# Optimization experiments

Measured on AMD Instinct MI355X. Metric: run time of the kernel, lower is better.

## Reference

```python
import jax, jax.numpy as jnp
import numpy as np

C = 64          # channels
HEADS = 4       # num_heads -> head_dim = 16
HID = int(C * 2.66)  # 170, GDFN hidden channels
B, H, W = 2, 256, 256


def conv1x1(x, w):
    # x: (b,c,h,w), w: (o,c) -> pointwise conv, no bias
    return jnp.einsum('bchw,oc->bohw', x, w)


def dwconv3x3(x, w):
    # depthwise 3x3, SAME padding; w: (C,1,3,3)
    return jax.lax.conv_general_dilated(
        x, w, window_strides=(1, 1), padding='SAME',
        feature_group_count=x.shape[1],
        dimension_numbers=('NCHW', 'OIHW', 'NCHW'))


def layer_norm_c(x, w, b):
    # torch: LayerNorm over channel dim of (b, hw, c), eps=1e-5
    mu = x.mean(axis=1, keepdims=True)
    var = ((x - mu) ** 2).mean(axis=1, keepdims=True)
    xn = (x - mu) / jnp.sqrt(var + 1e-5)
    return xn * w[None, :, None, None] + b[None, :, None, None]


def l2norm(x):
    # F.normalize(dim=-1), eps=1e-12
    n = jnp.sqrt(jnp.sum(x * x, axis=-1, keepdims=True))
    return x / jnp.maximum(n, 1e-12)


def mdta(x, temp, w_qkv, w_qkv_dw, w_po, w_kv, w_kv_dw, w_pof):
    b, c, h, w_ = x.shape
    d = c // HEADS
    qkv = dwconv3x3(conv1x1(x, w_qkv), w_qkv_dw)
    q, k, v = jnp.split(qkv, 3, axis=1)
    rs = lambda t: t.reshape(b, HEADS, d, h * w_)
    q, k, v = l2norm(rs(q)), l2norm(rs(k)), rs(v)
    # channel attention: (b,heads,d,d), softmax over last dim
    attn = jax.nn.softmax(jnp.einsum('bhdn,bhen->bhde', q, k) * temp, axis=-1)
    out = conv1x1(jnp.einsum('bhde,bhen->bhdn', attn, v).reshape(b, c, h, w_), w_po)
    # second gated branch: kv from `out`, reuse attn (qf/kf/attnf are dead code in source)
    kvf = dwconv3x3(conv1x1(out, w_kv), w_kv_dw)
    _kf, vf = jnp.split(kvf, 2, axis=1)
    vf = rs(vf)
    outf = conv1x1(jnp.einsum('bhde,bhen->bhdn', attn, vf).reshape(b, c, h, w_), w_pof)
    return outf


def gdfn(x, w_in, w_dw, w_out):
    x12 = dwconv3x3(conv1x1(x, w_in), w_dw)
    x1, x2 = jnp.split(x12, 2, axis=1)
    return conv1x1(jax.nn.gelu(x1, approximate=False) * x2, w_out)


def setup_inputs() -> dict:
    key = jax.random.key(0)
    ks = jax.random.split(key, 10)
    s = 0.05
    return {
        'x': jax.random.normal(ks[0], (B, C, H, W), jnp.float32),
        'n1_w': jnp.ones((C,), jnp.float32),
        'n1_b': jnp.zeros((C,), jnp.float32),
        'temp': jnp.ones((1, HEADS, 1, 1), jnp.float32),
        'w_qkv': jax.random.normal(ks[1], (3 * C, C), jnp.float32) * s,
        'w_qkv_dw': jax.random.normal(ks[2], (3 * C, 1, 3, 3), jnp.float32) * s,
        'w_po': jax.random.normal(ks[3], (C, C), jnp.float32) * s,
        'w_kv': jax.random.normal(ks[4], (2 * C, C), jnp.float32) * s,
        'w_kv_dw': jax.random.normal(ks[5], (2 * C, 1, 3, 3), jnp.float32) * s,
        'w_pof': jax.random.normal(ks[6], (C, C), jnp.float32) * s,
        'n2_w': jnp.ones((C,), jnp.float32),
        'n2_b': jnp.zeros((C,), jnp.float32),
        'w_in': jax.random.normal(ks[7], (2 * HID, C), jnp.float32) * s,
        'w_dw': jax.random.normal(ks[8], (2 * HID, 1, 3, 3), jnp.float32) * s,
        'w_out': jax.random.normal(ks[9], (C, HID), jnp.float32) * s,
    }


def reference(x, n1_w, n1_b, temp, w_qkv, w_qkv_dw, w_po, w_kv, w_kv_dw, w_pof,
              n2_w, n2_b, w_in, w_dw, w_out):
    x = x + mdta(layer_norm_c(x, n1_w, n1_b), temp,
                 w_qkv, w_qkv_dw, w_po, w_kv, w_kv_dw, w_pof)
    x = x + gdfn(layer_norm_c(x, n2_w, n2_b), w_in, w_dw, w_out)
    return x
```

## Files before the change

### kernel.cpp

```cpp
#include <hip/hip_runtime.h>
#include <hip/hip_bf16.h>
#include <math.h>

#define NPB 65536
#define BATCH 2
#define NTOT (BATCH * NPB)

typedef unsigned short u16;
typedef __attribute__((ext_vector_type(8))) short short8;
typedef __attribute__((ext_vector_type(4))) float f32x4;


__device__ __forceinline__ float bf2f(u16 u) {
  union { unsigned u; float f; } v; v.u = ((unsigned)u) << 16; return v.f;
}
__device__ __forceinline__ u16 f2bf(float f) {
  union { float f; unsigned u; } v; v.f = f;
  unsigned r = v.u + 0x7FFFu + ((v.u >> 16) & 1u);
  return (u16)(r >> 16);
}
__device__ __forceinline__ unsigned pk2(float a, float b) {
  return (unsigned)f2bf(a) | ((unsigned)f2bf(b) << 16);
}
__device__ __forceinline__ f32x4 mm(short8 a, short8 b, f32x4 c) {
  return __builtin_amdgcn_mfma_f32_16x16x32_bf16(a, b, c, 0, 0, 0);
}
__device__ __forceinline__ short8 ldfrag(const u16* F, int frag, int l) {
  return *reinterpret_cast<const short8*>(F + ((size_t)frag * 64 + l) * 8);
}
__device__ __forceinline__ void st4(u16* p, f32x4 c) {
  uint2 v; v.x = pk2(c[0], c[1]); v.y = pk2(c[2], c[3]);
  *reinterpret_cast<uint2*>(p) = v;
}
__device__ __forceinline__ float gelu_t(float a) {
  const float z = 0.7978845608f * fmaf(0.044715f * a, a * a, a);
  const float e = __expf(2.f * z);
  const float th = 1.f - 2.f / (e + 1.f);
  return 0.5f * a * (1.f + th);
}

__global__ __launch_bounds__(64) void k_wprep(
    const float* __restrict__ wqkv, const float* __restrict__ win,
    const float* __restrict__ wout, u16* __restrict__ WQf,
    u16* __restrict__ WIf, u16* __restrict__ WOf)
{
  const int f = blockIdx.x;
  const int l = threadIdx.x;
  const int fr = l & 15, fq = l >> 4;
  short8 v;
  u16* dst;
  if (f < 24) {
    const int t = f >> 1, kh = f & 1;
    const int row = t * 16 + fr;
#pragma unroll
    for (int j = 0; j < 8; ++j)
      v[j] = (short)f2bf(wqkv[(size_t)row * 64 + kh * 32 + fq * 8 + j]);
    dst = WQf + ((size_t)f * 64 + l) * 8;
  } else if (f < 68) {
    const int fi = f - 24;
    const int g = fi >> 1, kh = fi & 1;
    const int half = g / 11, t = g % 11;
    const int col = half * 176 + t * 16 + fr;
    const int row = col < 170 ? col : (col < 176 ? -1 : (col < 346 ? col - 6 : -1));
#pragma unroll
    for (int j = 0; j < 8; ++j)
      v[j] = (row < 0) ? (short)0
             : (short)f2bf(win[(size_t)row * 64 + kh * 32 + fq * 8 + j]);
    dst = WIf + ((size_t)fi * 64 + l) * 8;
  } else {
    const int fi = f - 68;
    const int t = fi / 6, kh = fi % 6;
    const int row = t * 16 + fr;
#pragma unroll
    for (int j = 0; j < 8; ++j) {
      const int k = kh * 32 + fq * 8 + j;
      v[j] = (k < 170) ? (short)f2bf(wout[(size_t)row * 170 + k]) : (short)0;
    }
    dst = WOf + ((size_t)fi * 64 + l) * 8;
  }
  *reinterpret_cast<short8*>(dst) = v;
}

__global__ __launch_bounds__(256, 4) void k_ln1(
    const float* __restrict__ x, const float* __restrict__ n1w,
    const float* __restrict__ n1b, u16* __restrict__ Y1)
{
  const int n = blockIdx.x * 256 + threadIdx.x;
  const int b = blockIdx.y;
  const size_t pix = (size_t)b * NPB + n;
  const float* xb = x + ((size_t)b * 64) * NPB + n;
  float y[64];
  float mu = 0.f;
#pragma unroll
  for (int c = 0; c < 64; ++c) { y[c] = xb[(size_t)c * NPB]; mu += y[c]; }
  mu *= (1.f / 64.f);
  float var = 0.f;
#pragma unroll
  for (int c = 0; c < 64; ++c) { float d = y[c] - mu; var = fmaf(d, d, var); }
  const float rstd = rsqrtf(var * (1.f / 64.f) + 1e-5f);
#pragma unroll
  for (int c = 0; c < 64; ++c) y[c] = (y[c] - mu) * rstd * n1w[c] + n1b[c];
#pragma unroll
  for (int cb = 0; cb < 4; ++cb) {
    u16* dst = Y1 + ((size_t)cb * NTOT + pix) * 16;
    uint4 v0, v1;
    v0.x = pk2(y[cb*16+0],  y[cb*16+1]);  v0.y = pk2(y[cb*16+2],  y[cb*16+3]);
    v0.z = pk2(y[cb*16+4],  y[cb*16+5]);  v0.w = pk2(y[cb*16+6],  y[cb*16+7]);
    v1.x = pk2(y[cb*16+8],  y[cb*16+9]);  v1.y = pk2(y[cb*16+10], y[cb*16+11]);
    v1.z = pk2(y[cb*16+12], y[cb*16+13]); v1.w = pk2(y[cb*16+14], y[cb*16+15]);
    *reinterpret_cast<uint4*>(dst) = v0;
    *reinterpret_cast<uint4*>(dst + 8) = v1;
  }
}

__global__ __launch_bounds__(256, 2) void g_qkvp(
    const u16* __restrict__ Y1, const u16* __restrict__ WQf,
    u16* __restrict__ qkvp)
{
  const int l = threadIdx.x & 63, fr = l & 15, fq = l >> 4;
  const int wv = blockIdx.x * 4 + (threadIdx.x >> 6);
  const int nw = gridDim.x * 4;
  short8 A[12][2];
#pragma unroll
  for (int t = 0; t < 12; ++t)
#pragma unroll
    for (int kh = 0; kh < 2; ++kh) A[t][kh] = ldfrag(WQf, t * 2 + kh, l);
  const size_t hof = (size_t)(fq & 1) * 8;
  for (int tile = wv; tile < 8192; tile += nw) {
    const size_t n = (size_t)tile * 16 + fr;
    const short8 b0 = *reinterpret_cast<const short8*>(
        Y1 + (((size_t)(fq >> 1)) * NTOT + n) * 16 + hof);
    const short8 b1 = *reinterpret_cast<const short8*>(
        Y1 + (((size_t)(2 + (fq >> 1))) * NTOT + n) * 16 + hof);
    f32x4 c[12];
#pragma unroll
    for (int t = 0; t < 12; ++t) c[t] = f32x4{0.f, 0.f, 0.f, 0.f};
#pragma unroll
    for (int t = 0; t < 12; ++t) c[t] = mm(A[t][0], b0, c[t]);
#pragma unroll
    for (int t = 0; t < 12; ++t) c[t] = mm(A[t][1], b1, c[t]);
#pragma unroll
    for (int t = 0; t < 12; ++t)
      st4(qkvp + ((size_t)t * NTOT + n) * 16 + fq * 4, c[t]);
  }
}

template<int CH, bool GATE, int STRIP>
__global__ __launch_bounds__(256, 2) void k_dwr(
    const u16* __restrict__ in, u16* __restrict__ out,
    const float* __restrict__ wdw, int wofs)
{
  typedef short __attribute__((ext_vector_type(CH))) shortC;
  constexpr int NPL = GATE ? 2 : 1;
  constexpr int LPP = 16 / CH;
  constexpr int NX  = 256 / LPP;
  constexpr int XC  = 256 / NX;
  const int t = threadIdx.x;
  const int sub = t % LPP, xi = t / LPP;
  const int q = blockIdx.x / XC, xc = blockIdx.x % XC;
  const int strip = blockIdx.y, b = blockIdx.z;
  const int x = xc * NX + xi;
  const int y0 = strip * STRIP;
  const int e0 = sub * CH;
  const int c0 = q * 16 + e0;

  const u16* pin[NPL];
  pin[0] = in + ((size_t)q * NTOT + (size_t)b * NPB) * 16 + e0;
  if (GATE)
    pin[NPL - 1] = in + ((size_t)(11 + q) * NTOT + (size_t)b * NPB) * 16 + e0;

  float w[NPL][9][CH];
#pragma unroll
  for (int pl = 0; pl < NPL; ++pl)
#pragma unroll
    for (int ch = 0; ch < CH; ++ch) {
      const int c = c0 + ch;
      int row; bool valid;
      if (GATE) { valid = c < 170; row = pl * 170 + c; }
      else { valid = true; row = wofs + c; }
#pragma unroll
      for (int tap = 0; tap < 9; ++tap)
        w[pl][tap][ch] = valid ? wdw[(size_t)row * 9 + tap] : 0.f;
    }

  auto LD = [&](const u16* p, int yy, int xx) -> shortC {
    shortC v;
#pragma unroll
    for (int j = 0; j < CH; ++j) v[j] = 0;
    if ((unsigned)yy < 256u && (unsigned)xx < 256u)
      v = *reinterpret_cast<const shortC*>(p + (size_t)(yy * 256 + xx) * 16);
    return v;
  };

  shortC r[NPL][3][3];
#pragma unroll
  for (int pl = 0; pl < NPL; ++pl) {
    r[pl][0][0] = LD(pin[pl], y0 - 1, x - 1);
    r[pl][0][1] = LD(pin[pl], y0 - 1, x);
    r[pl][0][2] = LD(pin[pl], y0 - 1, x + 1);
    r[pl][1][0] = LD(pin[pl], y0, x - 1);
    r[pl][1][1] = LD(pin[pl], y0, x);
    r[pl][1][2] = LD(pin[pl], y0, x + 1);
  }

#pragma unroll 2
  for (int yy = 0; yy < STRIP; ++yy) {
    const int y = y0 + yy;
#pragma unroll
    for (int pl = 0; pl < NPL; ++pl) {
      r[pl][2][0] = LD(pin[pl], y + 1, x - 1);
      r[pl][2][1] = LD(pin[pl], y + 1, x);
      r[pl][2][2] = LD(pin[pl], y + 1, x + 1);
    }
    float acc[NPL][CH];
#pragma unroll
    for (int pl = 0; pl < NPL; ++pl)
#pragma unroll
      for (int ch = 0; ch < CH; ++ch) acc[pl][ch] = 0.f;
#pragma unroll
    for (int pl = 0; pl < NPL; ++pl)
#pragma unroll
      for (int ky = 0; ky < 3; ++ky)
#pragma unroll
        for (int kx = 0; kx < 3; ++kx)
#pragma unroll
          for (int ch = 0; ch < CH; ++ch)
            acc[pl][ch] = fmaf(w[pl][ky * 3 + kx][ch],
                               bf2f((u16)r[pl][ky][kx][ch]), acc[pl][ch]);

    float v[CH];
#pragma unroll
    for (int ch = 0; ch < CH; ++ch) {
      if (GATE) {
        v[ch] = gelu_t(acc[0][ch]) * acc[NPL - 1][ch];
      } else {
        v[ch] = acc[0][ch];
      }
    }
    u16* po = out + ((size_t)q * NTOT + (size_t)b * NPB +
                     (size_t)(y * 256 + x)) * 16 + e0;
    if constexpr (CH == 4) {
      uint2 o; o.x = pk2(v[0], v[1]); o.y = pk2(v[2], v[3]);
      *reinterpret_cast<uint2*>(po) = o;
    } else {
      uint4 o;
      o.x = pk2(v[0], v[1]); o.y = pk2(v[2], v[3]);
      o.z = pk2(v[4], v[5]); o.w = pk2(v[6], v[7]);
      *reinterpret_cast<uint4*>(po) = o;
    }
#pragma unroll
    for (int pl = 0; pl < NPL; ++pl)
#pragma unroll
      for (int dx = 0; dx < 3; ++dx) {
        r[pl][0][dx] = r[pl][1][dx];
        r[pl][1][dx] = r[pl][2][dx];
      }
  }
}

__global__ __launch_bounds__(256, 2) void k_gram_p(
    const u16* __restrict__ qkv, float* __restrict__ part)
{
  __shared__ __align__(16) u16 lds[32][520];
  const int chunk = blockIdx.x, h = blockIdx.y, b = blockIdx.z;
  const int t = threadIdx.x;
#pragma unroll
  for (int i = 0; i < 2; ++i) {
    const int p = t + i * 256;
    const size_t pix = (size_t)b * NPB + chunk * 512 + p;
    const u16* srcq = qkv + ((size_t)h * NTOT + pix) * 16;
    const u16* srck = qkv + ((size_t)(4 + h) * NTOT + pix) * 16;
    const short8 q0 = *reinterpret_cast<const short8*>(srcq);
    const short8 q1 = *reinterpret_cast<const short8*>(srcq + 8);
    const short8 k0 = *reinterpret_cast<const short8*>(srck);
    const short8 k1 = *reinterpret_cast<const short8*>(srck + 8);
#pragma unroll
    for (int j = 0; j < 8; ++j) {
      lds[j][p] = (u16)q0[j];  lds[8 + j][p] = (u16)q1[j];
      lds[16 + j][p] = (u16)k0[j]; lds[24 + j][p] = (u16)k1[j];
    }
  }
  __syncthreads();
  const int w = t >> 6, l = t & 63, fr = l & 15, fq = l >> 4;
  if (w >= 3) return;
  float* pp = part + ((size_t)((b * 4 + h) * 128) + chunk) * 288;
  const int rowA = (w == 2) ? 16 + fr : fr;
  const int rowB = (w == 0) ? 16 + fr : rowA;
  f32x4 acc = {0.f, 0.f, 0.f, 0.f};
#pragma unroll
  for (int kt = 0; kt < 16; ++kt) {
    const short8 a  = *reinterpret_cast<const short8*>(&lds[rowA][kt * 32 + fq * 8]);
    const short8 bb = *reinterpret_cast<const short8*>(&lds[rowB][kt * 32 + fq * 8]);
    acc = mm(a, bb, acc);
  }
  if (w == 0) {
#pragma unroll
    for (int r = 0; r < 4; ++r) pp[(fq * 4 + r) * 16 + fr] = acc[r];
  } else if ((fr >> 2) == fq) {
    pp[(w == 1 ? 256 : 272) + fr] = acc[fr & 3];
  }
}

__global__ __launch_bounds__(320) void k_gram_red(
    const float* __restrict__ part, float* __restrict__ G,
    float* __restrict__ Sq, float* __restrict__ Sk)
{
  const int bh = blockIdx.x;
  const int t = threadIdx.x;
  if (t >= 288) return;
  const float* p = part + (size_t)bh * 128 * 288 + t;
  float s = 0.f;
  for (int ch = 0; ch < 128; ++ch) s += p[(size_t)ch * 288];
  const int b = bh >> 2, h = bh & 3;
  if (t < 256) G[bh * 256 + t] = s;
  else if (t < 272) Sq[b * 64 + h * 16 + (t - 256)] = s;
  else Sk[b * 64 + h * 16 + (t - 272)] = s;
}

__global__ __launch_bounds__(256) void k_attn(
    const float* __restrict__ G, const float* __restrict__ Sq,
    const float* __restrict__ Sk, const float* __restrict__ temp,
    const float* __restrict__ wpo, const float* __restrict__ wkv,
    const float* __restrict__ wpof, u16* __restrict__ Pf,
    u16* __restrict__ M2f)
{
  __shared__ float attn[BATCH][4][16][16];
  __shared__ float M1[BATCH][64][64];
  __shared__ float rq[128], rk[128];
  const int t = threadIdx.x;
  if (t < 128) {
    rq[t] = 1.f / fmaxf(sqrtf(Sq[t]), 1e-12f);
    rk[t] = 1.f / fmaxf(sqrtf(Sk[t]), 1e-12f);
  }
  __syncthreads();
  if (t < 128) {
    const int b = t >> 6, h = (t >> 4) & 3, d = t & 15;
    const float tm = temp[h];
    const float* g = G + ((b * 4 + h) * 16 + d) * 16;
    const float rqd = rq[b * 64 + h * 16 + d];
    float L[16], mx = -1e30f;
#pragma unroll
    for (int e = 0; e < 16; ++e) {
      L[e] = g[e] * rqd * rk[b * 64 + h * 16 + e] * tm;
      mx = fmaxf(mx, L[e]);
    }
    float s = 0.f;
#pragma unroll
    for (int e = 0; e < 16; ++e) { L[e] = expf(L[e] - mx); s += L[e]; }
    const float inv = 1.f / s;
#pragma unroll
    for (int e = 0; e < 16; ++e) attn[b][h][d][e] = L[e] * inv;
  }
  __syncthreads();
  for (int s0 = 0; s0 < 32; ++s0) {
    const int idx = t * 32 + s0;
    const int b = idx >> 12, o = (idx >> 6) & 63, c = idx & 63;
    const int h = c >> 4, e = c & 15;
    float a = 0.f;
#pragma unroll
    for (int d = 0; d < 16; ++d) a = fmaf(wpo[o * 64 + h * 16 + d], attn[b][h][d][e], a);
    M1[b][o][c] = a;
  }
  __syncthreads();
  for (int it = 0; it < 4; ++it) {
    const int idx = it * 256 + t;
    const int l = idx & 63;
    const int fi = idx >> 6;
    const int b = fi >> 3, tt = (fi >> 1) & 3, kh = fi & 1;
    const int fr = l & 15, fq = l >> 4;
    const int o = tt * 16 + fr;
    short8 pv, mv;
#pragma unroll
    for (int j = 0; j < 8; ++j) {
      const int c = kh * 32 + fq * 8 + j;
      const int h = c >> 4, e = c & 15;
      float a2 = 0.f;
#pragma unroll
      for (int d = 0; d < 16; ++d)
        a2 = fmaf(wpof[o * 64 + h * 16 + d], attn[b][h][d][e], a2);
      mv[j] = (short)f2bf(a2);
      float a = 0.f;
      for (int jj = 0; jj < 64; ++jj)
        a = fmaf(wkv[(64 + o) * 64 + jj], M1[b][jj][c], a);
      pv[j] = (short)f2bf(a);
    }
    *reinterpret_cast<short8*>(Pf + ((size_t)fi * 64 + l) * 8) = pv;
    *reinterpret_cast<short8*>(M2f + ((size_t)fi * 64 + l) * 8) = mv;
  }
}

__global__ __launch_bounds__(256, 2) void g_pv(
    const u16* __restrict__ qkv, const u16* __restrict__ Pf,
    u16* __restrict__ vfp)
{
  const int l = threadIdx.x & 63, fr = l & 15, fq = l >> 4;
  const int wv = blockIdx.x * 4 + (threadIdx.x >> 6);
  const int nw = gridDim.x * 4;
  const int b = blockIdx.z;
  short8 A[4][2];
#pragma unroll
  for (int t = 0; t < 4; ++t)
#pragma unroll
    for (int kh = 0; kh < 2; ++kh)
      A[t][kh] = ldfrag(Pf, (b * 4 + t) * 2 + kh, l);
  const size_t hof = (size_t)(fq & 1) * 8;
  for (int tile = wv; tile < 4096; tile += nw) {
    const size_t n = (size_t)b * NPB + (size_t)tile * 16 + fr;
    const short8 b0 = *reinterpret_cast<const short8*>(
        qkv + ((size_t)(8 + (fq >> 1)) * NTOT + n) * 16 + hof);
    const short8 b1 = *reinterpret_cast<const short8*>(
        qkv + ((size_t)(10 + (fq >> 1)) * NTOT + n) * 16 + hof);
    f32x4 c[4];
#pragma unroll
    for (int t = 0; t < 4; ++t) c[t] = f32x4{0.f, 0.f, 0.f, 0.f};
#pragma unroll
    for (int t = 0; t < 4; ++t) c[t] = mm(A[t][0], b0, c[t]);
#pragma unroll
    for (int t = 0; t < 4; ++t) c[t] = mm(A[t][1], b1, c[t]);
#pragma unroll
    for (int t = 0; t < 4; ++t)
      st4(vfp + ((size_t)t * NTOT + n) * 16 + fq * 4, c[t]);
  }
}

__global__ __launch_bounds__(256, 2) void g_x2ln(
    const u16* __restrict__ vf, const u16* __restrict__ M2f,
    const float* __restrict__ x, const float* __restrict__ n2w,
    const float* __restrict__ n2b, u16* __restrict__ X2,
    u16* __restrict__ Y2)
{
  const int l = threadIdx.x & 63, fr = l & 15, fq = l >> 4;
  const int wv = blockIdx.x * 4 + (threadIdx.x >> 6);
  const int nw = gridDim.x * 4;
  const int b = blockIdx.z;
  short8 A[4][2];
#pragma unroll
  for (int t = 0; t < 4; ++t)
#pragma unroll
    for (int kh = 0; kh < 2; ++kh)
      A[t][kh] = ldfrag(M2f, (b * 4 + t) * 2 + kh, l);
  const size_t hof = (size_t)(fq & 1) * 8;
  for (int tile = wv; tile < 4096; tile += nw) {
    const int pix0 = tile * 16;
    const size_t n = (size_t)b * NPB + pix0 + fr;
    const short8 b0 = *reinterpret_cast<const short8*>(
        vf + ((size_t)(fq >> 1) * NTOT + n) * 16 + hof);
    const short8 b1 = *reinterpret_cast<const short8*>(
        vf + ((size_t)(2 + (fq >> 1)) * NTOT + n) * 16 + hof);
    f32x4 c[4];
#pragma unroll
    for (int t = 0; t < 4; ++t) c[t] = f32x4{0.f, 0.f, 0.f, 0.f};
#pragma unroll
    for (int t = 0; t < 4; ++t) c[t] = mm(A[t][0], b0, c[t]);
#pragma unroll
    for (int t = 0; t < 4; ++t) c[t] = mm(A[t][1], b1, c[t]);
    const int pix = pix0 + fr;
#pragma unroll
    for (int t = 0; t < 4; ++t)
#pragma unroll
      for (int r = 0; r < 4; ++r)
        c[t][r] += x[((size_t)(b * 64 + t * 16 + fq * 4 + r)) * NPB + pix];
#pragma unroll
    for (int t = 0; t < 4; ++t)
      st4(X2 + ((size_t)t * NTOT + n) * 16 + fq * 4, c[t]);
    float s = 0.f;
#pragma unroll
    for (int t = 0; t < 4; ++t)
#pragma unroll
      for (int r = 0; r < 4; ++r) s += c[t][r];
    s += __shfl_xor(s, 16); s += __shfl_xor(s, 32);
    const float mu = s * (1.f / 64.f);
    float ss = 0.f;
#pragma unroll
    for (int t = 0; t < 4; ++t)
#pragma unroll
      for (int r = 0; r < 4; ++r) { float d = c[t][r] - mu; ss = fmaf(d, d, ss); }
    ss += __shfl_xor(ss, 16); ss += __shfl_xor(ss, 32);
    const float rstd = rsqrtf(ss * (1.f / 64.f) + 1e-5f);
#pragma unroll
    for (int t = 0; t < 4; ++t)
#pragma unroll
      for (int r = 0; r < 4; ++r) {
        const int oc = t * 16 + fq * 4 + r;
        c[t][r] = (c[t][r] - mu) * rstd * n2w[oc] + n2b[oc];
      }
#pragma unroll
    for (int t = 0; t < 4; ++t)
      st4(Y2 + ((size_t)t * NTOT + n) * 16 + fq * 4, c[t]);
  }
}

__global__ __launch_bounds__(256, 2) void g_win(
    const u16* __restrict__ Y2, const u16* __restrict__ WIf,
    u16* __restrict__ hpre)
{
  const int l = threadIdx.x & 63, fr = l & 15, fq = l >> 4;
  const int wv = blockIdx.x * 4 + (threadIdx.x >> 6);
  const int nw = gridDim.x * 4;
  const int half = wv & 1;
  short8 A[11][2];
#pragma unroll
  for (int t = 0; t < 11; ++t)
#pragma unroll
    for (int kh = 0; kh < 2; ++kh)
      A[t][kh] = ldfrag(WIf, (half * 11 + t) * 2 + kh, l);
  const size_t hof = (size_t)(fq & 1) * 8;
  for (int tile = wv >> 1; tile < 8192; tile += (nw >> 1)) {
    const size_t n = (size_t)tile * 16 + fr;
    const short8 b0 = *reinterpret_cast<const short8*>(
        Y2 + ((size_t)(fq >> 1) * NTOT + n) * 16 + hof);
    const short8 b1 = *reinterpret_cast<const short8*>(
        Y2 + ((size_t)(2 + (fq >> 1)) * NTOT + n) * 16 + hof);
    f32x4 c[11];
#pragma unroll
    for (int t = 0; t < 11; ++t) c[t] = f32x4{0.f, 0.f, 0.f, 0.f};
#pragma unroll
    for (int t = 0; t < 11; ++t) c[t] = mm(A[t][0], b0, c[t]);
#pragma unroll
    for (int t = 0; t < 11; ++t) c[t] = mm(A[t][1], b1, c[t]);
#pragma unroll
    for (int t = 0; t < 11; ++t)
      st4(hpre + ((size_t)(half * 11 + t) * NTOT + n) * 16 + fq * 4, c[t]);
  }
}

__global__ __launch_bounds__(256, 2) void g_out(
    const u16* __restrict__ hg, const u16* __restrict__ WOf,
    const u16* __restrict__ X2, float* __restrict__ out)
{
  const int l = threadIdx.x & 63, fr = l & 15, fq = l >> 4;
  const int wv = blockIdx.x * 4 + (threadIdx.x >> 6);
  const int nw = gridDim.x * 4;
  short8 A[4][6];
#pragma unroll
  for (int t = 0; t < 4; ++t)
#pragma unroll
    for (int kh = 0; kh < 6; ++kh)
      A[t][kh] = ldfrag(WOf, t * 6 + kh, l);
  const size_t hof = (size_t)(fq & 1) * 8;
  for (int tile = wv; tile < 8192; tile += nw) {
    const size_t n = (size_t)tile * 16 + fr;
    short8 bb[6];
#pragma unroll
    for (int kh = 0; kh < 6; ++kh) {
      int hb = kh * 2 + (fq >> 1);
      if (hb > 10) hb = 10;
      bb[kh] = *reinterpret_cast<const short8*>(
          hg + ((size_t)hb * NTOT + n) * 16 + hof);
    }
    f32x4 c[4];
#pragma unroll
    for (int t = 0; t < 4; ++t) c[t] = f32x4{0.f, 0.f, 0.f, 0.f};
#pragma unroll
    for (int kh = 0; kh < 6; ++kh)
#pragma unroll
      for (int t = 0; t < 4; ++t) c[t] = mm(A[t][kh], bb[kh], c[t]);
    const int b = (int)(n >> 16);
    const int pix = (int)(n & 65535);
#pragma unroll
    for (int t = 0; t < 4; ++t) {
      const uint2 xv = *reinterpret_cast<const uint2*>(
          X2 + ((size_t)t * NTOT + n) * 16 + fq * 4);
      const u16 h0 = (u16)(xv.x & 0xffff), h1 = (u16)(xv.x >> 16);
      const u16 h2 = (u16)(xv.y & 0xffff), h3 = (u16)(xv.y >> 16);
      const int ocb = b * 64 + t * 16 + fq * 4;
      out[((size_t)(ocb + 0)) * NPB + pix] = c[t][0] + bf2f(h0);
      out[((size_t)(ocb + 1)) * NPB + pix] = c[t][1] + bf2f(h1);
      out[((size_t)(ocb + 2)) * NPB + pix] = c[t][2] + bf2f(h2);
      out[((size_t)(ocb + 3)) * NPB + pix] = c[t][3] + bf2f(h3);
    }
  }
}

extern "C" void kernel_launch(void* const* d_in, const int* in_sizes, int n_in,
                              void* d_out, int out_size, void* d_ws, size_t ws_size,
                              hipStream_t stream)
{
  const float* x     = (const float*)d_in[0];
  const float* n1w   = (const float*)d_in[1];
  const float* n1b   = (const float*)d_in[2];
  const float* temp  = (const float*)d_in[3];
  const float* wqkv  = (const float*)d_in[4];
  const float* wqkvd = (const float*)d_in[5];
  const float* wpo   = (const float*)d_in[6];
  const float* wkv   = (const float*)d_in[7];
  const float* wkvd  = (const float*)d_in[8];
  const float* wpof  = (const float*)d_in[9];
  const float* n2w   = (const float*)d_in[10];
  const float* n2b   = (const float*)d_in[11];
  const float* win   = (const float*)d_in[12];
  const float* wdw   = (const float*)d_in[13];
  const float* wout  = (const float*)d_in[14];
  float* out = (float*)d_out;

  char* ws = (char*)d_ws;
  const size_t offA  = 0;
  const size_t offB  = 16777216;
  const size_t offC  = offB + 50331648;
  const size_t offHg = offC + 50331648;
  const size_t offX2 = offHg + 46137344 + 256;
  const size_t offSm = offX2 + 16777216;

  u16* Y1   = (u16*)(ws + offA);
  u16* VFP  = (u16*)(ws + offA);
  u16* Y2   = (u16*)(ws + offA);
  u16* QKVp = (u16*)(ws + offB);
  u16* VF   = (u16*)(ws + offB);
  u16* Hpre = (u16*)(ws + offB);
  u16* QKV  = (u16*)(ws + offC);
  u16* Hg   = (u16*)(ws + offHg);
  u16* X2   = (u16*)(ws + offX2);
  float* part = (float*)(ws + offSm);
  float* G    = (float*)(ws + offSm + 1179648);
  float* Sq   = (float*)(ws + offSm + 1179648 + 8192);
  float* Sk   = (float*)(ws + offSm + 1179648 + 8704);
  u16* Pf     = (u16*)(ws + offSm + 1179648 + 9216);
  u16* M2f    = (u16*)(ws + offSm + 1179648 + 25600);
  u16* WQf    = (u16*)(ws + offSm + 1179648 + 41984);
  u16* WIf    = (u16*)(ws + offSm + 1179648 + 66560);
  u16* WOf    = (u16*)(ws + offSm + 1179648 + 111616);

  k_wprep<<<dim3(92), 64, 0, stream>>>(wqkv, win, wout, WQf, WIf, WOf);
  k_ln1<<<dim3(NPB / 256, BATCH), 256, 0, stream>>>(x, n1w, n1b, Y1);
  g_qkvp<<<dim3(512), 256, 0, stream>>>(Y1, WQf, QKVp);
  k_dwr<8, false, 16><<<dim3(24, 16, BATCH), 256, 0, stream>>>(QKVp, QKV, wqkvd, 0);
  k_gram_p<<<dim3(128, 4, BATCH), 256, 0, stream>>>(QKV, part);
  k_gram_red<<<dim3(BATCH * 4), 320, 0, stream>>>(part, G, Sq, Sk);
  k_attn<<<dim3(1), 256, 0, stream>>>(G, Sq, Sk, temp, wpo, wkv, wpof, Pf, M2f);
  g_pv<<<dim3(256, 1, BATCH), 256, 0, stream>>>(QKV, Pf, VFP);
  k_dwr<8, false, 8><<<dim3(8, 32, BATCH), 256, 0, stream>>>(VFP, VF, wkvd, 64);
  g_x2ln<<<dim3(256, 1, BATCH), 256, 0, stream>>>(VF, M2f, x, n2w, n2b, X2, Y2);
  g_win<<<dim3(512), 256, 0, stream>>>(Y2, WIf, Hpre);
  k_dwr<4, true, 16><<<dim3(44, 16, BATCH), 256, 0, stream>>>(Hpre, Hg, wdw, 0);
  g_out<<<dim3(512), 256, 0, stream>>>(Hg, WOf, X2, out);
}
```

Before: 244.6 us.

## Fuse GDFN input 1x1 conv with depthwise 3x3 and GELU gate in LDS tiles

Replaces the separate g_win pointwise conv and gated depthwise conv kernels with one kernel. Each block loads a 16x16 spatial tile plus halo of Y2 into LDS, computes the hidden channels per 16-channel group with MFMA into LDS, then applies the 3x3 depthwise conv and GELU gate directly. This removes the large Hpre round trip through global memory (340 bf16 channels written then re-read with halo). In exchange it recomputes the halo pixels' pointwise conv, rounds depthwise weights to bf16, and uses a large LDS footprint, which may limit occupancy.

```diff
diff --git a/kernel.cpp b/kernel.cpp
--- a/kernel.cpp
+++ b/kernel.cpp
@@ -8,6 +8,7 @@
 
 typedef unsigned short u16;
 typedef __attribute__((ext_vector_type(8))) short short8;
+typedef __attribute__((ext_vector_type(4))) short short4v;
 typedef __attribute__((ext_vector_type(4))) float f32x4;
 
 
@@ -145,13 +146,12 @@
   }
 }
 
-template<int CH, bool GATE, int STRIP>
+template<int CH, int STRIP>
 __global__ __launch_bounds__(256, 2) void k_dwr(
     const u16* __restrict__ in, u16* __restrict__ out,
     const float* __restrict__ wdw, int wofs)
 {
   typedef short __attribute__((ext_vector_type(CH))) shortC;
-  constexpr int NPL = GATE ? 2 : 1;
   constexpr int LPP = 16 / CH;
   constexpr int NX  = 256 / LPP;
   constexpr int XC  = 256 / NX;
@@ -164,97 +164,161 @@
   const int e0 = sub * CH;
   const int c0 = q * 16 + e0;
 
-  const u16* pin[NPL];
-  pin[0] = in + ((size_t)q * NTOT + (size_t)b * NPB) * 16 + e0;
-  if (GATE)
-    pin[NPL - 1] = in + ((size_t)(11 + q) * NTOT + (size_t)b * NPB) * 16 + e0;
-
-  float w[NPL][9][CH];
-#pragma unroll
-  for (int pl = 0; pl < NPL; ++pl)
-#pragma unroll
-    for (int ch = 0; ch < CH; ++ch) {
-      const int c = c0 + ch;
-      int row; bool valid;
-      if (GATE) { valid = c < 170; row = pl * 170 + c; }
-      else { valid = true; row = wofs + c; }
-#pragma unroll
-      for (int tap = 0; tap < 9; ++tap)
-        w[pl][tap][ch] = valid ? wdw[(size_t)row * 9 + tap] : 0.f;
-    }
-
-  auto LD = [&](const u16* p, int yy, int xx) -> shortC {
+  const u16* pin = in + ((size_t)q * NTOT + (size_t)b * NPB) * 16 + e0;
+
+  float w[9][CH];
+#pragma unroll
+  for (int ch = 0; ch < CH; ++ch) {
+    const int row = wofs + c0 + ch;
+#pragma unroll
+    for (int tap = 0; tap < 9; ++tap)
+      w[tap][ch] = wdw[(size_t)row * 9 + tap];
+  }
+
+  auto LD = [&](int yy, int xx) -> shortC {
     shortC v;
 #pragma unroll
     for (int j = 0; j < CH; ++j) v[j] = 0;
     if ((unsigned)yy < 256u && (unsigned)xx < 256u)
-      v = *reinterpret_cast<const shortC*>(p + (size_t)(yy * 256 + xx) * 16);
+      v = *reinterpret_cast<const shortC*>(pin + (size_t)(yy * 256 + xx) * 16);
     return v;
   };
 
-  shortC r[NPL][3][3];
-#pragma unroll
-  for (int pl = 0; pl < NPL; ++pl) {
-    r[pl][0][0] = LD(pin[pl], y0 - 1, x - 1);
-    r[pl][0][1] = LD(pin[pl], y0 - 1, x);
-    r[pl][0][2] = LD(pin[pl], y0 - 1, x + 1);
-    r[pl][1][0] = LD(pin[pl], y0, x - 1);
-    r[pl][1][1] = LD(pin[pl], y0, x);
-    r[pl][1][2] = LD(pin[pl], y0, x + 1);
-  }
+  shortC r[3][3];
+  r[0][0] = LD(y0 - 1, x - 1); r[0][1] = LD(y0 - 1, x); r[0][2] = LD(y0 - 1, x + 1);
+  r[1][0] = LD(y0, x - 1);     r[1][1] = LD(y0, x);     r[1][2] = LD(y0, x + 1);
 
 #pragma unroll 2
   for (int yy = 0; yy < STRIP; ++yy) {
     const int y = y0 + yy;
-#pragma unroll
-    for (int pl = 0; pl < NPL; ++pl) {
-      r[pl][2][0] = LD(pin[pl], y + 1, x - 1);
-      r[pl][2][1] = LD(pin[pl], y + 1, x);
-      r[pl][2][2] = LD(pin[pl], y + 1, x + 1);
-    }
-    float acc[NPL][CH];
-#pragma unroll
-    for (int pl = 0; pl < NPL; ++pl)
-#pragma unroll
-      for (int ch = 0; ch < CH; ++ch) acc[pl][ch] = 0.f;
-#pragma unroll
-    for (int pl = 0; pl < NPL; ++pl)
-#pragma unroll
-      for (int ky = 0; ky < 3; ++ky)
-#pragma unroll
-        for (int kx = 0; kx < 3; ++kx)
-#pragma unroll
-          for (int ch = 0; ch < CH; ++ch)
-            acc[pl][ch] = fmaf(w[pl][ky * 3 + kx][ch],
-                               bf2f((u16)r[pl][ky][kx][ch]), acc[pl][ch]);
-
-    float v[CH];
-#pragma unroll
-    for (int ch = 0; ch < CH; ++ch) {
-      if (GATE) {
-        v[ch] = gelu_t(acc[0][ch]) * acc[NPL - 1][ch];
-      } else {
-        v[ch] = acc[0][ch];
-      }
-    }
+    r[2][0] = LD(y + 1, x - 1); r[2][1] = LD(y + 1, x); r[2][2] = LD(y + 1, x + 1);
+    float acc[CH];
+#pragma unroll
+    for (int ch = 0; ch < CH; ++ch) acc[ch] = 0.f;
+#pragma unroll
+    for (int ky = 0; ky < 3; ++ky)
+#pragma unroll
+      for (int kx = 0; kx < 3; ++kx)
+#pragma unroll
+        for (int ch = 0; ch < CH; ++ch)
+          acc[ch] = fmaf(w[ky * 3 + kx][ch], bf2f((u16)r[ky][kx][ch]), acc[ch]);
     u16* po = out + ((size_t)q * NTOT + (size_t)b * NPB +
                      (size_t)(y * 256 + x)) * 16 + e0;
-    if constexpr (CH == 4) {
+    uint4 o;
+    o.x = pk2(acc[0], acc[1]); o.y = pk2(acc[2], acc[3]);
+    o.z = pk2(acc[4], acc[5]); o.w = pk2(acc[6], acc[7]);
+    *reinterpret_cast<uint4*>(po) = o;
+#pragma unroll
+    for (int dx = 0; dx < 3; ++dx) { r[0][dx] = r[1][dx]; r[1][dx] = r[2][dx]; }
+  }
+}
+
+__global__ __launch_bounds__(256, 2) void g_windwg(
+    const u16* __restrict__ Y2, const u16* __restrict__ WIf,
+    const float* __restrict__ wdw, u16* __restrict__ Hg)
+{
+  __shared__ __align__(16) u16 sy[336 * 72];
+  __shared__ __align__(16) u16 sh[336 * 36];
+  __shared__ __align__(16) u16 swt[2 * 9 * 176];
+  const int t = threadIdx.x;
+  const int tx0 = blockIdx.x * 16, ty0 = blockIdx.y * 16;
+  const int b = blockIdx.z;
+  const size_t bofs = (size_t)b * NPB;
+
+  for (int i = t; i < 2 * 9 * 176; i += 256) {
+    const int pl = i / (9 * 176);
+    const int r = i % (9 * 176);
+    const int tap = r / 176, c = r % 176;
+    swt[i] = (c < 170) ? f2bf(wdw[((size_t)(pl * 170 + c)) * 9 + tap]) : (u16)0;
+  }
+  for (int idx = t; idx < 336; idx += 256) {
+    const int py = idx / 18, px = idx % 18;
+    const int gy = ty0 + py - 1, gx = tx0 + px - 1;
+    const bool ok = (idx < 324) && ((unsigned)gy < 256u) && ((unsigned)gx < 256u);
+#pragma unroll
+    for (int cb = 0; cb < 4; ++cb) {
+      short8 v0, v1;
+      if (ok) {
+        const u16* src = Y2 + ((size_t)cb * NTOT + bofs + (size_t)(gy * 256 + gx)) * 16;
+        v0 = *reinterpret_cast<const short8*>(src);
+        v1 = *reinterpret_cast<const short8*>(src + 8);
+      } else {
+#pragma unroll
+        for (int j = 0; j < 8; ++j) { v0[j] = 0; v1[j] = 0; }
+      }
+      *reinterpret_cast<short8*>(&sy[idx * 72 + cb * 16]) = v0;
+      *reinterpret_cast<short8*>(&sy[idx * 72 + cb * 16 + 8]) = v1;
+    }
+  }
+  __syncthreads();
+
+  const int w = t >> 6, l = t & 63, fr = l & 15, fq = l >> 4;
+  const int sub = t & 3, colx = (t >> 2) & 15, rg = t >> 6;
+  const int e0 = sub * 4;
+
+  for (int q = 0; q < 11; ++q) {
+    const short8 a10 = ldfrag(WIf, q * 2, l);
+    const short8 a11 = ldfrag(WIf, q * 2 + 1, l);
+    const short8 a20 = ldfrag(WIf, (11 + q) * 2, l);
+    const short8 a21 = ldfrag(WIf, (11 + q) * 2 + 1, l);
+    for (int i = w; i < 21; i += 4) {
+      const u16* sp = &sy[(i * 16 + fr) * 72];
+      const short8 b0 = *reinterpret_cast<const short8*>(sp + fq * 8);
+      const short8 b1 = *reinterpret_cast<const short8*>(sp + 32 + fq * 8);
+      f32x4 c1 = {0.f, 0.f, 0.f, 0.f}, c2 = {0.f, 0.f, 0.f, 0.f};
+      c1 = mm(a10, b0, c1); c1 = mm(a11, b1, c1);
+      c2 = mm(a20, b0, c2); c2 = mm(a21, b1, c2);
+      u16* dp = &sh[(i * 16 + fr) * 36];
+      st4(dp + fq * 4, c1);
+      st4(dp + 16 + fq * 4, c2);
+    }
+    __syncthreads();
+
+    float wf[2][9][4];
+#pragma unroll
+    for (int pl = 0; pl < 2; ++pl)
+#pragma unroll
+      for (int tap = 0; tap < 9; ++tap) {
+        const short4v wv = *reinterpret_cast<const short4v*>(
+            &swt[(pl * 9 + tap) * 176 + q * 16 + e0]);
+#pragma unroll
+        for (int j = 0; j < 4; ++j) wf[pl][tap][j] = bf2f((u16)wv[j]);
+      }
+    short4v rwin[3][3][2];
+    auto LDR = [&](int hr, int slot) {
+#pragma unroll
+      for (int dx = 0; dx < 3; ++dx)
+#pragma unroll
+        for (int pl = 0; pl < 2; ++pl)
+          rwin[slot][dx][pl] = *reinterpret_cast<const short4v*>(
+              &sh[(hr * 18 + colx + dx) * 36 + pl * 16 + e0]);
+    };
+    const int r0 = rg * 4;
+    LDR(r0, 0); LDR(r0 + 1, 1);
+#pragma unroll
+    for (int k = 0; k < 4; ++k) {
+      LDR(r0 + k + 2, (k + 2) % 3);
+      const int s0 = k % 3, s1 = (k + 1) % 3, s2 = (k + 2) % 3;
+      float acc[2][4] = {{0.f, 0.f, 0.f, 0.f}, {0.f, 0.f, 0.f, 0.f}};
+#pragma unroll
+      for (int pl = 0; pl < 2; ++pl)
+#pragma unroll
+        for (int dx = 0; dx < 3; ++dx)
+#pragma unroll
+          for (int j = 0; j < 4; ++j) {
+            acc[pl][j] = fmaf(wf[pl][0 + dx][j], bf2f((u16)rwin[s0][dx][pl][j]), acc[pl][j]);
+            acc[pl][j] = fmaf(wf[pl][3 + dx][j], bf2f((u16)rwin[s1][dx][pl][j]), acc[pl][j]);
+            acc[pl][j] = fmaf(wf[pl][6 + dx][j], bf2f((u16)rwin[s2][dx][pl][j]), acc[pl][j]);
+          }
+      float v[4];
+#pragma unroll
+      for (int j = 0; j < 4; ++j) v[j] = gelu_t(acc[0][j]) * acc[1][j];
+      const int gy = ty0 + r0 + k, gx = tx0 + colx;
       uint2 o; o.x = pk2(v[0], v[1]); o.y = pk2(v[2], v[3]);
-      *reinterpret_cast<uint2*>(po) = o;
-    } else {
-      uint4 o;
-      o.x = pk2(v[0], v[1]); o.y = pk2(v[2], v[3]);
-      o.z = pk2(v[4], v[5]); o.w = pk2(v[6], v[7]);
-      *reinterpret_cast<uint4*>(po) = o;
-    }
-#pragma unroll
-    for (int pl = 0; pl < NPL; ++pl)
-#pragma unroll
-      for (int dx = 0; dx < 3; ++dx) {
-        r[pl][0][dx] = r[pl][1][dx];
-        r[pl][1][dx] = r[pl][2][dx];
-      }
+      *reinterpret_cast<uint2*>(
+          Hg + ((size_t)q * NTOT + bofs + (size_t)(gy * 256 + gx)) * 16 + e0) = o;
+    }
+    __syncthreads();
   }
 }
 
@@ -487,40 +551,6 @@
 #pragma unroll
     for (int t = 0; t < 4; ++t)
       st4(Y2 + ((size_t)t * NTOT + n) * 16 + fq * 4, c[t]);
-  }
-}
-
-__global__ __launch_bounds__(256, 2) void g_win(
-    const u16* __restrict__ Y2, const u16* __restrict__ WIf,
-    u16* __restrict__ hpre)
-{
-  const int l = threadIdx.x & 63, fr = l & 15, fq = l >> 4;
-  const int wv = blockIdx.x * 4 + (threadIdx.x >> 6);
-  const int nw = gridDim.x * 4;
-  const int half = wv & 1;
-  short8 A[11][2];
-#pragma unroll
-  for (int t = 0; t < 11; ++t)
-#pragma unroll
-    for (int kh = 0; kh < 2; ++kh)
-      A[t][kh] = ldfrag(WIf, (half * 11 + t) * 2 + kh, l);
-  const size_t hof = (size_t)(fq & 1) * 8;
-  for (int tile = wv >> 1; tile < 8192; tile += (nw >> 1)) {
-    const size_t n = (size_t)tile * 16 + fr;
-    const short8 b0 = *reinterpret_cast<const short8*>(
-        Y2 + ((size_t)(fq >> 1) * NTOT + n) * 16 + hof);
-    const short8 b1 = *reinterpret_cast<const short8*>(
-        Y2 + ((size_t)(2 + (fq >> 1)) * NTOT + n) * 16 + hof);
-    f32x4 c[11];
-#pragma unroll
-    for (int t = 0; t < 11; ++t) c[t] = f32x4{0.f, 0.f, 0.f, 0.f};
-#pragma unroll
-    for (int t = 0; t < 11; ++t) c[t] = mm(A[t][0], b0, c[t]);
-#pragma unroll
-    for (int t = 0; t < 11; ++t) c[t] = mm(A[t][1], b1, c[t]);
-#pragma unroll
-    for (int t = 0; t < 11; ++t)
-      st4(hpre + ((size_t)(half * 11 + t) * NTOT + n) * 16 + fq * 4, c[t]);
   }
 }
 
@@ -606,7 +636,6 @@
   u16* Y2   = (u16*)(ws + offA);
   u16* QKVp = (u16*)(ws + offB);
   u16* VF   = (u16*)(ws + offB);
-  u16* Hpre = (u16*)(ws + offB);
   u16* QKV  = (u16*)(ws + offC);
   u16* Hg   = (u16*)(ws + offHg);
   u16* X2   = (u16*)(ws + offX2);
@@ -623,14 +652,13 @@
   k_wprep<<<dim3(92), 64, 0, stream>>>(wqkv, win, wout, WQf, WIf, WOf);
   k_ln1<<<dim3(NPB / 256, BATCH), 256, 0, stream>>>(x, n1w, n1b, Y1);
   g_qkvp<<<dim3(512), 256, 0, stream>>>(Y1, WQf, QKVp);
-  k_dwr<8, false, 16><<<dim3(24, 16, BATCH), 256, 0, stream>>>(QKVp, QKV, wqkvd, 0);
+  k_dwr<8, 16><<<dim3(24, 16, BATCH), 256, 0, stream>>>(QKVp, QKV, wqkvd, 0);
   k_gram_p<<<dim3(128, 4, BATCH), 256, 0, stream>>>(QKV, part);
   k_gram_red<<<dim3(BATCH * 4), 320, 0, stream>>>(part, G, Sq, Sk);
   k_attn<<<dim3(1), 256, 0, stream>>>(G, Sq, Sk, temp, wpo, wkv, wpof, Pf, M2f);
   g_pv<<<dim3(256, 1, BATCH), 256, 0, stream>>>(QKV, Pf, VFP);
-  k_dwr<8, false, 8><<<dim3(8, 32, BATCH), 256, 0, stream>>>(VFP, VF, wkvd, 64);
+  k_dwr<8, 8><<<dim3(8, 32, BATCH), 256, 0, stream>>>(VFP, VF, wkvd, 64);
   g_x2ln<<<dim3(256, 1, BATCH), 256, 0, stream>>>(VF, M2f, x, n2w, n2b, X2, Y2);
-  g_win<<<dim3(512), 256, 0, stream>>>(Y2, WIf, Hpre);
-  k_dwr<4, true, 16><<<dim3(44, 16, BATCH), 256, 0, stream>>>(Hpre, Hg, wdw, 0);
+  g_windwg<<<dim3(16, 16, BATCH), 256, 0, stream>>>(Y2, WIf, wdw, Hg);
   g_out<<<dim3(512), 256, 0, stream>>>(Hg, WOf, X2, out);
 }
```

Result: faster. 232.5 us (-4.9%).
